# Kernel optimization log

Hardware: AMD Instinct MI355X
Metric: run time of the kernel (lower is better)

## Reference

```python
import jax, jax.numpy as jnp
import numpy as np

N_NODES = 50000
N_HEDGES = 10000
NNZ_INC = 400000
NNZ_E = 80000
NNZ_V = 400000
VDIM = 128
EDIM = 128
OUT_VDIM = 128
OUT_EDIM = 128


def _spmm(rows, cols, vals, X, n_rows):
    # sparse COO [n_rows, n_cols] @ X  -> [n_rows, d]
    return jax.ops.segment_sum(vals[:, None] * X[cols], rows, num_segments=n_rows)


def setup_inputs() -> dict:
    key = jax.random.key(0)
    ks = jax.random.split(key, 20)
    inp = {
        "vfeat": jax.random.normal(ks[0], (N_NODES, VDIM), jnp.float32),
        "efeat": jax.random.normal(ks[1], (N_HEDGES, EDIM), jnp.float32),
        "invDV": jax.random.uniform(ks[2], (N_NODES,), jnp.float32),
        "invDE": jax.random.uniform(ks[3], (N_HEDGES,), jnp.float32),
        "inc_src": jax.random.randint(ks[4], (NNZ_INC,), 0, N_NODES, jnp.int32),
        "inc_dst": jax.random.randint(ks[5], (NNZ_INC,), 0, N_HEDGES, jnp.int32),
        "emat_rows": jax.random.randint(ks[6], (NNZ_E,), 0, N_HEDGES, jnp.int32),
        "emat_cols": jax.random.randint(ks[7], (NNZ_E,), 0, N_HEDGES, jnp.int32),
        "emat_vals": jax.random.normal(ks[8], (NNZ_E,), jnp.float32),
        "vmat_rows": jax.random.randint(ks[9], (NNZ_V,), 0, N_NODES, jnp.int32),
        "vmat_cols": jax.random.randint(ks[10], (NNZ_V,), 0, N_NODES, jnp.int32),
        "vmat_vals": jax.random.normal(ks[11], (NNZ_V,), jnp.float32),
        # parameters (torch Linear: y = x @ W.T + b)
        "Wv": jax.random.normal(ks[12], (OUT_VDIM, VDIM), jnp.float32) * 0.05,
        "We": jax.random.normal(ks[13], (OUT_EDIM, EDIM), jnp.float32) * 0.05,
        "psi1_W": jax.random.normal(ks[14], (VDIM, VDIM + EDIM), jnp.float32) * 0.05,
        "psi1_b": jnp.zeros((VDIM,), jnp.float32),
        "psi2_W": jax.random.normal(ks[15], (EDIM, OUT_VDIM + EDIM), jnp.float32) * 0.05,
        "psi2_b": jnp.zeros((EDIM,), jnp.float32),
    }
    return inp


def reference(vfeat, efeat, invDV, invDE, inc_src, inc_dst,
              emat_rows, emat_cols, emat_vals,
              vmat_rows, vmat_cols, vmat_vals,
              Wv, We, psi1_W, psi1_b, psi2_W, psi2_b):
    N = vfeat.shape[0]
    E = efeat.shape[0]
    # --- 'in' update_all with psi1: per-incidence concat -> linear -> *invDV[src] -> sum into hyperedge
    x = jnp.concatenate([vfeat[inc_src], efeat[inc_dst]], axis=1)  # [nnz, VDIM+EDIM]
    x = x @ psi1_W.T + psi1_b                                       # [nnz, VDIM]
    x = x * invDV[inc_src][:, None]
    A = jax.ops.segment_sum(x, inc_dst, num_segments=E)             # [E, VDIM]
    A = _spmm(emat_rows, emat_cols, emat_vals, A, E)
    _efeat = A + efeat
    # --- 'con' update_all: node gathers sum of incident hyperedge feats
    _vfeat = jax.ops.segment_sum(_efeat[inc_dst], inc_src, num_segments=N)
    vfeat_out = jax.nn.relu(_vfeat @ Wv.T)                           # [N, OUT_VDIM]
    # --- 'in' update_all with psi2 (dv = ones)
    x2 = jnp.concatenate([vfeat_out[inc_src], efeat[inc_dst]], axis=1)
    x2 = x2 @ psi2_W.T + psi2_b                                      # [nnz, EDIM]
    B = jax.ops.segment_sum(x2, inc_dst, num_segments=E) * invDE[:, None]
    # --- 'con' pass with efeat, then vMat spmm, then 'in' sum back to hyperedges
    _vfeat2 = jax.ops.segment_sum(efeat[inc_dst], inc_src, num_segments=N)
    _vfeat2 = _spmm(vmat_rows, vmat_cols, vmat_vals, _vfeat2, N)
    _efeat2 = jax.ops.segment_sum(_vfeat2[inc_src], inc_dst, num_segments=E)
    _efeat2 = _efeat2 + B
    efeat_out = jax.nn.relu(_efeat2 @ We.T)                          # [E, OUT_EDIM]
    return vfeat_out, efeat_out
```

## Files before the change

### kernel.cpp

```cpp
#include <hip/hip_runtime.h>

#define NN 50000
#define NE 10000
#define NNZ_INC 400000
#define NNZ_E 80000
#define NNZ_V 400000
#define D 128
#define KC 32

#define CAP_D 112
#define CAP_S 40
#define CAP_E 40
#define CAP_V 40

#define NE_SH (NE / 8)
#define NN_SH (NN / 8)

#define GE_ 157
#define G_HINC ((NNZ_INC + 255) / 256)
#define G_HIST8 (8 * G_HINC)
#define G_EVB ((NNZ_E + NNZ_V + 255) / 256)
#define G_CVTN 6250
#define G_CVTE 1250
#define G_NR16 (NN / 16)
#define G_ER16 (NE / 16)

typedef unsigned short u16;
typedef unsigned int u32;

__device__ __forceinline__ u16 f2bf(float x) {
    unsigned u = __float_as_uint(x);
    unsigned r = u + 0x7fffu + ((u >> 16) & 1u);
    return (u16)(r >> 16);
}
__device__ __forceinline__ float bf2f(u16 h) {
    return __uint_as_float(((unsigned)h) << 16);
}

__device__ __forceinline__ void acc8(uint4 u, float acc[8]) {
    acc[0] += __uint_as_float(u.x << 16);
    acc[1] += __uint_as_float(u.x & 0xffff0000u);
    acc[2] += __uint_as_float(u.y << 16);
    acc[3] += __uint_as_float(u.y & 0xffff0000u);
    acc[4] += __uint_as_float(u.z << 16);
    acc[5] += __uint_as_float(u.z & 0xffff0000u);
    acc[6] += __uint_as_float(u.w << 16);
    acc[7] += __uint_as_float(u.w & 0xffff0000u);
}
__device__ __forceinline__ void fma8(uint4 u, float v, float acc[8]) {
    acc[0] = fmaf(v, __uint_as_float(u.x << 16), acc[0]);
    acc[1] = fmaf(v, __uint_as_float(u.x & 0xffff0000u), acc[1]);
    acc[2] = fmaf(v, __uint_as_float(u.y << 16), acc[2]);
    acc[3] = fmaf(v, __uint_as_float(u.y & 0xffff0000u), acc[3]);
    acc[4] = fmaf(v, __uint_as_float(u.z << 16), acc[4]);
    acc[5] = fmaf(v, __uint_as_float(u.z & 0xffff0000u), acc[5]);
    acc[6] = fmaf(v, __uint_as_float(u.w << 16), acc[6]);
    acc[7] = fmaf(v, __uint_as_float(u.w & 0xffff0000u), acc[7]);
}
__device__ __forceinline__ uint4 pack_bf8(const float acc[8]) {
    uint4 o;
    o.x = (u32)f2bf(acc[0]) | ((u32)f2bf(acc[1]) << 16);
    o.y = (u32)f2bf(acc[2]) | ((u32)f2bf(acc[3]) << 16);
    o.z = (u32)f2bf(acc[4]) | ((u32)f2bf(acc[5]) << 16);
    o.w = (u32)f2bf(acc[6]) | ((u32)f2bf(acc[7]) << 16);
    return o;
}

__device__ __forceinline__ void gemm_acc(
    int bx, const float* __restrict__ X, const float* __restrict__ W, int ldw,
    int M, float acc[8][4])
{
    __shared__ float XsT[KC][68];
    __shared__ float Ws[KC][132];
    const int tid = threadIdx.x;
    const int tx = tid & 31, ty = tid >> 5;
    const int row0 = bx * 64;
    const int c0 = tx * 4;
    const int r0 = ty * 8;

#pragma unroll
    for (int r = 0; r < 8; ++r)
#pragma unroll
        for (int c = 0; c < 4; ++c) acc[r][c] = 0.f;

    for (int kc = 0; kc < D; kc += KC) {
        __syncthreads();
#pragma unroll
        for (int it = 0; it < 2; ++it) {
            int l = tid + it * 256;
            int r = l >> 3, k4 = l & 7;
            float4 v = make_float4(0.f, 0.f, 0.f, 0.f);
            int row = row0 + r;
            if (row < M) v = ((const float4*)(X + (size_t)row * D + kc))[k4];
            int k = k4 * 4;
            XsT[k + 0][r] = v.x; XsT[k + 1][r] = v.y;
            XsT[k + 2][r] = v.z; XsT[k + 3][r] = v.w;
        }
#pragma unroll
        for (int it = 0; it < 4; ++it) {
            int l = tid + it * 256;
            int o = l >> 3, k4 = l & 7;
            float4 w = ((const float4*)(W + (size_t)o * ldw + kc))[k4];
            int k = k4 * 4;
            Ws[k + 0][o] = w.x; Ws[k + 1][o] = w.y;
            Ws[k + 2][o] = w.z; Ws[k + 3][o] = w.w;
        }
        __syncthreads();
#pragma unroll
        for (int k = 0; k < KC; ++k) {
            const float4 a0 = *(const float4*)&XsT[k][r0];
            const float4 a1 = *(const float4*)&XsT[k][r0 + 4];
            const float4 b  = *(const float4*)&Ws[k][c0];
            float av[8] = {a0.x, a0.y, a0.z, a0.w, a1.x, a1.y, a1.z, a1.w};
            float bv[4] = {b.x, b.y, b.z, b.w};
#pragma unroll
            for (int r = 0; r < 8; ++r)
#pragma unroll
                for (int c = 0; c < 4; ++c)
                    acc[r][c] = fmaf(av[r], bv[c], acc[r][c]);
        }
    }
}

__global__ __launch_bounds__(256) void mega0(
    const int* __restrict__ inc_src, const int* __restrict__ inc_dst,
    int* __restrict__ cnt_dst, int* __restrict__ cnt_src,
    u16* __restrict__ ell_d, u16* __restrict__ ell_s,
    const int* __restrict__ erows, const int* __restrict__ ecols,
    const float* __restrict__ evals, int* __restrict__ cnt_e, u32* __restrict__ ev_e,
    const int* __restrict__ vrows, const int* __restrict__ vcols,
    const float* __restrict__ vvals, int* __restrict__ cnt_v, u32* __restrict__ ev_v,
    const float* __restrict__ efeat, const float* __restrict__ vfeat,
    const float* __restrict__ invDV,
    u16* __restrict__ vfi_b, u16* __restrict__ efeat_b)
{
    int b = blockIdx.x;
    if (b < G_HIST8) {
        int shard = b & 7;
        int i = (b >> 3) * 256 + threadIdx.x;
        if (i < NNZ_INC) {
            int s = inc_src[i], d = inc_dst[i];
            if ((u32)(d - shard * NE_SH) < (u32)NE_SH) {
                int rd = atomicAdd(cnt_dst + d, 1);
                if (rd < CAP_D) ell_d[d * CAP_D + rd] = (u16)s;
            }
            if ((u32)(s - shard * NN_SH) < (u32)NN_SH) {
                int rs = atomicAdd(cnt_src + s, 1);
                if (rs < CAP_S) ell_s[s * CAP_S + rs] = (u16)d;
            }
        }
    } else if (b < G_HIST8 + G_EVB) {
        int i = (b - G_HIST8) * 256 + threadIdx.x;
        if (i < NNZ_E) {
            int r = erows[i];
            int re = atomicAdd(cnt_e + r, 1);
            if (re < CAP_E)
                ev_e[r * CAP_E + re] = ((u32)ecols[i] << 16) | (u32)f2bf(evals[i]);
        } else if (i < NNZ_E + NNZ_V) {
            int j = i - NNZ_E;
            int r = vrows[j];
            int rv = atomicAdd(cnt_v + r, 1);
            if (rv < CAP_V)
                ev_v[r * CAP_V + rv] = ((u32)vcols[j] << 16) | (u32)f2bf(vvals[j]);
        }
    } else if (b < G_HIST8 + G_EVB + G_CVTN) {
        int i = ((b - G_HIST8 - G_EVB) * 256 + threadIdx.x) * 4;
        int row = i >> 7;
        float s = invDV[row];
        float4 v = *(const float4*)(vfeat + i);
        ushort4 u;
        u.x = f2bf(v.x * s); u.y = f2bf(v.y * s);
        u.z = f2bf(v.z * s); u.w = f2bf(v.w * s);
        *(ushort4*)(vfi_b + i) = u;
    } else {
        int i = ((b - G_HIST8 - G_EVB - G_CVTN) * 256 + threadIdx.x) * 4;
        float4 v = *(const float4*)(efeat + i);
        ushort4 u;
        u.x = f2bf(v.x); u.y = f2bf(v.y); u.z = f2bf(v.z); u.w = f2bf(v.w);
        *(ushort4*)(efeat_b + i) = u;
    }
}

__device__ __forceinline__ void segsum_bf_ell16(int rb,
    const int* __restrict__ cnt, int cap, const u16* __restrict__ ell,
    const u16* __restrict__ Tb, u16* __restrict__ Yb, int R)
{
    int r = rb * 16 + (threadIdx.x >> 4);
    int q = threadIdx.x & 15;
    if (r >= R) return;
    int m = min(cnt[r], cap);
    const u16* lst = ell + (size_t)r * cap;
    float acc[8] = {0.f, 0.f, 0.f, 0.f, 0.f, 0.f, 0.f, 0.f};
    int j = 0;
    for (; j + 3 < m; j += 4) {
        ushort4 ix = *(const ushort4*)(lst + j);
        uint4 u0 = *(const uint4*)(Tb + (size_t)ix.x * D + q * 8);
        uint4 u1 = *(const uint4*)(Tb + (size_t)ix.y * D + q * 8);
        uint4 u2 = *(const uint4*)(Tb + (size_t)ix.z * D + q * 8);
        uint4 u3 = *(const uint4*)(Tb + (size_t)ix.w * D + q * 8);
        acc8(u0, acc); acc8(u1, acc); acc8(u2, acc); acc8(u3, acc);
    }
    for (; j < m; ++j) {
        uint4 u0 = *(const uint4*)(Tb + (size_t)lst[j] * D + q * 8);
        acc8(u0, acc);
    }
    ((uint4*)(Yb + (size_t)r * D))[q] = pack_bf8(acc);
}

__device__ __forceinline__ void segsum_f_ell16(int rb,
    const int* __restrict__ cnt, int cap, const u16* __restrict__ ell,
    const u16* __restrict__ Tb, float* __restrict__ Y, int R)
{
    int r = rb * 16 + (threadIdx.x >> 4);
    int q = threadIdx.x & 15;
    if (r >= R) return;
    int m = min(cnt[r], cap);
    const u16* lst = ell + (size_t)r * cap;
    float acc[8] = {0.f, 0.f, 0.f, 0.f, 0.f, 0.f, 0.f, 0.f};
    int j = 0;
    for (; j + 7 < m; j += 8) {
        ushort4 ixa = *(const ushort4*)(lst + j);
        ushort4 ixb = *(const ushort4*)(lst + j + 4);
        uint4 u0 = *(const uint4*)(Tb + (size_t)ixa.x * D + q * 8);
        uint4 u1 = *(const uint4*)(Tb + (size_t)ixa.y * D + q * 8);
        uint4 u2 = *(const uint4*)(Tb + (size_t)ixa.z * D + q * 8);
        uint4 u3 = *(const uint4*)(Tb + (size_t)ixa.w * D + q * 8);
        uint4 u4 = *(const uint4*)(Tb + (size_t)ixb.x * D + q * 8);
        uint4 u5 = *(const uint4*)(Tb + (size_t)ixb.y * D + q * 8);
        uint4 u6 = *(const uint4*)(Tb + (size_t)ixb.z * D + q * 8);
        uint4 u7 = *(const uint4*)(Tb + (size_t)ixb.w * D + q * 8);
        acc8(u0, acc); acc8(u1, acc); acc8(u2, acc); acc8(u3, acc);
        acc8(u4, acc); acc8(u5, acc); acc8(u6, acc); acc8(u7, acc);
    }
    for (; j + 3 < m; j += 4) {
        ushort4 ix = *(const ushort4*)(lst + j);
        uint4 u0 = *(const uint4*)(Tb + (size_t)ix.x * D + q * 8);
        uint4 u1 = *(const uint4*)(Tb + (size_t)ix.y * D + q * 8);
        uint4 u2 = *(const uint4*)(Tb + (size_t)ix.z * D + q * 8);
        uint4 u3 = *(const uint4*)(Tb + (size_t)ix.w * D + q * 8);
        acc8(u0, acc); acc8(u1, acc); acc8(u2, acc); acc8(u3, acc);
    }
    for (; j < m; ++j) {
        uint4 u0 = *(const uint4*)(Tb + (size_t)lst[j] * D + q * 8);
        acc8(u0, acc);
    }
    float* yr = Y + (size_t)r * D;
    ((float4*)yr)[2 * q + 0] = make_float4(acc[0], acc[1], acc[2], acc[3]);
    ((float4*)yr)[2 * q + 1] = make_float4(acc[4], acc[5], acc[6], acc[7]);
}

__device__ __forceinline__ void spmm_bf_ell16(int rb,
    const int* __restrict__ cnt, int cap, const u32* __restrict__ ell,
    const u16* __restrict__ Xb, const float* __restrict__ addend,
    u16* __restrict__ Yb, int R)
{
    int r = rb * 16 + (threadIdx.x >> 4);
    int q = threadIdx.x & 15;
    if (r >= R) return;
    int m = min(cnt[r], cap);
    const u32* lst = ell + (size_t)r * cap;
    float acc[8];
    if (addend) {
        const float* ar = addend + (size_t)r * D;
        float4 lo = ((const float4*)ar)[2 * q + 0];
        float4 hi = ((const float4*)ar)[2 * q + 1];
        acc[0] = lo.x; acc[1] = lo.y; acc[2] = lo.z; acc[3] = lo.w;
        acc[4] = hi.x; acc[5] = hi.y; acc[6] = hi.z; acc[7] = hi.w;
    } else {
#pragma unroll
        for (int i = 0; i < 8; ++i) acc[i] = 0.f;
    }
    int j = 0;
    for (; j + 3 < m; j += 4) {
        uint4 e = *(const uint4*)(lst + j);
        uint4 x0 = *(const uint4*)(Xb + (size_t)(e.x >> 16) * D + q * 8);
        uint4 x1 = *(const uint4*)(Xb + (size_t)(e.y >> 16) * D + q * 8);
        uint4 x2 = *(const uint4*)(Xb + (size_t)(e.z >> 16) * D + q * 8);
        uint4 x3 = *(const uint4*)(Xb + (size_t)(e.w >> 16) * D + q * 8);
        fma8(x0, __uint_as_float(e.x << 16), acc);
        fma8(x1, __uint_as_float(e.y << 16), acc);
        fma8(x2, __uint_as_float(e.z << 16), acc);
        fma8(x3, __uint_as_float(e.w << 16), acc);
    }
    for (; j < m; ++j) {
        u32 e = lst[j];
        uint4 x = *(const uint4*)(Xb + (size_t)(e >> 16) * D + q * 8);
        fma8(x, __uint_as_float(e << 16), acc);
    }
    ((uint4*)(Yb + (size_t)r * D))[q] = pack_bf8(acc);
}

__global__ __launch_bounds__(256) void fusedA(
    const float* __restrict__ efeat,
    const float* __restrict__ psi2_W, const float* __restrict__ psi2_b, float* __restrict__ QeP,
    const float* __restrict__ Wv, float* __restrict__ efP,
    const int* __restrict__ cnt_dst, const u16* __restrict__ ell_d,
    const float* __restrict__ invDV, const u16* __restrict__ vfi_b,
    float* __restrict__ sva, float* __restrict__ wsum,
    const int* __restrict__ cnt_src, const u16* __restrict__ ell_s,
    const u16* __restrict__ efeat_b, u16* __restrict__ vf2_b)
{
    int b = blockIdx.x;
    if (b < GE_) {
        float acc[8][4];
        gemm_acc(b, efeat, psi2_W + D, 2 * D, NE, acc);
        int tx = threadIdx.x & 31, ty = threadIdx.x >> 5;
        float4 b4 = ((const float4*)psi2_b)[tx];
#pragma unroll
        for (int r = 0; r < 8; ++r) {
            int row = b * 64 + ty * 8 + r;
            if (row < NE) {
                float4 v = make_float4(acc[r][0] + b4.x, acc[r][1] + b4.y,
                                       acc[r][2] + b4.z, acc[r][3] + b4.w);
                ((float4*)(QeP + (size_t)row * D))[tx] = v;
            }
        }
    } else if (b < 2 * GE_) {
        int bx = b - GE_;
        float acc[8][4];
        gemm_acc(bx, efeat, Wv, D, NE, acc);
        int tx = threadIdx.x & 31, ty = threadIdx.x >> 5;
#pragma unroll
        for (int r = 0; r < 8; ++r) {
            int row = bx * 64 + ty * 8 + r;
            if (row < NE) {
                float4 v = make_float4(acc[r][0], acc[r][1], acc[r][2], acc[r][3]);
                ((float4*)(efP + (size_t)row * D))[tx] = v;
            }
        }
    } else if (b < 2 * GE_ + G_ER16) {
        int e = (b - 2 * GE_) * 16 + (threadIdx.x >> 4);
        int q = threadIdx.x & 15;
        if (e >= NE) return;
        int m = min(cnt_dst[e], CAP_D);
        const u16* lst = ell_d + (size_t)e * CAP_D;
        float acc[8] = {0.f, 0.f, 0.f, 0.f, 0.f, 0.f, 0.f, 0.f};
        float ws = 0.f;
        int j = 0;
        for (; j + 3 < m; j += 4) {
            ushort4 ix = *(const ushort4*)(lst + j);
            uint4 u0 = *(const uint4*)(vfi_b + (size_t)ix.x * D + q * 8);
            uint4 u1 = *(const uint4*)(vfi_b + (size_t)ix.y * D + q * 8);
            uint4 u2 = *(const uint4*)(vfi_b + (size_t)ix.z * D + q * 8);
            uint4 u3 = *(const uint4*)(vfi_b + (size_t)ix.w * D + q * 8);
            ws += (invDV[ix.x] + invDV[ix.y]) + (invDV[ix.z] + invDV[ix.w]);
            acc8(u0, acc); acc8(u1, acc); acc8(u2, acc); acc8(u3, acc);
        }
        for (; j < m; ++j) {
            int s = lst[j];
            uint4 u0 = *(const uint4*)(vfi_b + (size_t)s * D + q * 8);
            ws += invDV[s];
            acc8(u0, acc);
        }
        float* yr = sva + (size_t)e * D;
        ((float4*)yr)[2 * q + 0] = make_float4(acc[0], acc[1], acc[2], acc[3]);
        ((float4*)yr)[2 * q + 1] = make_float4(acc[4], acc[5], acc[6], acc[7]);
        if (q == 0) wsum[e] = ws;
    } else {
        segsum_bf_ell16(b - 2 * GE_ - G_ER16, cnt_src, CAP_S, ell_s, efeat_b, vf2_b, NN);
    }
}

__global__ __launch_bounds__(256) void fusedB2(
    const float* __restrict__ sva, const float* __restrict__ efeat,
    const float* __restrict__ wsum,
    const float* __restrict__ psi1_W, const float* __restrict__ psi1_b,
    const float* __restrict__ Wv, u16* __restrict__ AP_b,
    const int* __restrict__ cnt_v, const u32* __restrict__ ev_v,
    const u16* __restrict__ vf2_b, u16* __restrict__ vf2b_b)
{
    int b = blockIdx.x;
    if (b >= GE_) {
        spmm_bf_ell16(b - GE_, cnt_v, CAP_V, ev_v, vf2_b, nullptr, vf2b_b, NN);
        return;
    }
    __shared__ float XsT[KC][68];
    __shared__ float Ws[KC][132];
    const int bx = b;
    const int tid = threadIdx.x;
    const int tx = tid & 31, ty = tid >> 5;
    const int row0 = bx * 64;
    const int c0 = tx * 4;
    const int r0 = ty * 8;
    float acc[8][4];
#pragma unroll
    for (int r = 0; r < 8; ++r)
#pragma unroll
        for (int c = 0; c < 4; ++c) acc[r][c] = 0.f;

    for (int kc = 0; kc < 2 * D; kc += KC) {
        __syncthreads();
        const bool second = (kc >= D);
        const float* Xp = second ? efeat : sva;
        const int kk = second ? kc - D : kc;
#pragma unroll
        for (int it = 0; it < 2; ++it) {
            int l = tid + it * 256;
            int r = l >> 3, k4 = l & 7;
            float4 v = make_float4(0.f, 0.f, 0.f, 0.f);
            int row = row0 + r;
            if (row < NE) {
                v = ((const float4*)(Xp + (size_t)row * D + kk))[k4];
                if (second) {
                    float sc = wsum[row];
                    v.x *= sc; v.y *= sc; v.z *= sc; v.w *= sc;
                }
            }
            int k = k4 * 4;
            XsT[k + 0][r] = v.x; XsT[k + 1][r] = v.y;
            XsT[k + 2][r] = v.z; XsT[k + 3][r] = v.w;
        }
#pragma unroll
        for (int it = 0; it < 4; ++it) {
            int l = tid + it * 256;
            int o = l >> 3, k4 = l & 7;
            float4 w = ((const float4*)(psi1_W + (size_t)o * (2 * D) + kc))[k4];
            int k = k4 * 4;
            Ws[k + 0][o] = w.x; Ws[k + 1][o] = w.y;
            Ws[k + 2][o] = w.z; Ws[k + 3][o] = w.w;
        }
        __syncthreads();
#pragma unroll
        for (int k = 0; k < KC; ++k) {
            const float4 a0 = *(const float4*)&XsT[k][r0];
            const float4 a1 = *(const float4*)&XsT[k][r0 + 4];
            const float4 bb = *(const float4*)&Ws[k][c0];
            float av[8] = {a0.x, a0.y, a0.z, a0.w, a1.x, a1.y, a1.z, a1.w};
            float bv[4] = {bb.x, bb.y, bb.z, bb.w};
#pragma unroll
            for (int r = 0; r < 8; ++r)
#pragma unroll
                for (int c = 0; c < 4; ++c)
                    acc[r][c] = fmaf(av[r], bv[c], acc[r][c]);
        }
    }
    float4 b4 = ((const float4*)psi1_b)[tx];
    float wsv[8];
#pragma unroll
    for (int r = 0; r < 8; ++r) {
        int row = row0 + r0 + r;
        wsv[r] = (row < NE) ? wsum[row] : 0.f;
    }
    float accP[8][4];
#pragma unroll
    for (int r = 0; r < 8; ++r)
#pragma unroll
        for (int c = 0; c < 4; ++c) accP[r][c] = 0.f;

    for (int kc = 0; kc < D; kc += KC) {
        __syncthreads();
        if ((u32)(tx - (kc >> 2)) < 8u) {
            int kk0 = tx * 4 - kc;
#pragma unroll
            for (int r = 0; r < 8; ++r) {
                XsT[kk0 + 0][r0 + r] = fmaf(wsv[r], b4.x, acc[r][0]);
                XsT[kk0 + 1][r0 + r] = fmaf(wsv[r], b4.y, acc[r][1]);
                XsT[kk0 + 2][r0 + r] = fmaf(wsv[r], b4.z, acc[r][2]);
                XsT[kk0 + 3][r0 + r] = fmaf(wsv[r], b4.w, acc[r][3]);
            }
        }
#pragma unroll
        for (int it = 0; it < 4; ++it) {
            int l = tid + it * 256;
            int o = l >> 3, k4 = l & 7;
            float4 w = ((const float4*)(Wv + (size_t)o * D + kc))[k4];
            int k = k4 * 4;
            Ws[k + 0][o] = w.x; Ws[k + 1][o] = w.y;
            Ws[k + 2][o] = w.z; Ws[k + 3][o] = w.w;
        }
        __syncthreads();
#pragma unroll
        for (int k = 0; k < KC; ++k) {
            const float4 a0 = *(const float4*)&XsT[k][r0];
            const float4 a1 = *(const float4*)&XsT[k][r0 + 4];
            const float4 bb = *(const float4*)&Ws[k][c0];
            float av[8] = {a0.x, a0.y, a0.z, a0.w, a1.x, a1.y, a1.z, a1.w};
            float bv[4] = {bb.x, bb.y, bb.z, bb.w};
#pragma unroll
            for (int r = 0; r < 8; ++r)
#pragma unroll
                for (int c = 0; c < 4; ++c)
                    accP[r][c] = fmaf(av[r], bv[c], accP[r][c]);
        }
    }
#pragma unroll
    for (int r = 0; r < 8; ++r) {
        int row = row0 + r0 + r;
        if (row < NE) {
            ushort4 u;
            u.x = f2bf(accP[r][0]); u.y = f2bf(accP[r][1]);
            u.z = f2bf(accP[r][2]); u.w = f2bf(accP[r][3]);
            ((ushort4*)(AP_b + (size_t)row * D))[tx] = u;
        }
    }
}

__global__ __launch_bounds__(256) void fusedC2(
    const int* __restrict__ cnt_dst, const u16* __restrict__ ell_d,
    const u16* __restrict__ vf2b_b, float* __restrict__ av,
    const int* __restrict__ cnt_e, const u32* __restrict__ ev_e,
    const u16* __restrict__ AP_b, const float* __restrict__ efP, u16* __restrict__ A2P_b)
{
    int b = blockIdx.x;
    if (b < G_ER16) segsum_f_ell16(b, cnt_dst, CAP_D, ell_d, vf2b_b, av, NE);
    else spmm_bf_ell16(b - G_ER16, cnt_e, CAP_E, ev_e, AP_b, efP, A2P_b, NE);
}

__global__ __launch_bounds__(256) void outv_k(
    const int* __restrict__ cnt_src, const u16* __restrict__ ell_s,
    const u16* __restrict__ A2P_b, float* __restrict__ out_v, u16* __restrict__ outv_b)
{
    int r = blockIdx.x * 16 + (threadIdx.x >> 4);
    int q = threadIdx.x & 15;
    if (r >= NN) return;
    int m = min(cnt_src[r], CAP_S);
    const u16* lst = ell_s + (size_t)r * CAP_S;
    float acc[8] = {0.f, 0.f, 0.f, 0.f, 0.f, 0.f, 0.f, 0.f};
    int j = 0;
    for (; j + 3 < m; j += 4) {
        ushort4 ix = *(const ushort4*)(lst + j);
        uint4 u0 = *(const uint4*)(A2P_b + (size_t)ix.x * D + q * 8);
        uint4 u1 = *(const uint4*)(A2P_b + (size_t)ix.y * D + q * 8);
        uint4 u2 = *(const uint4*)(A2P_b + (size_t)ix.z * D + q * 8);
        uint4 u3 = *(const uint4*)(A2P_b + (size_t)ix.w * D + q * 8);
        acc8(u0, acc); acc8(u1, acc); acc8(u2, acc); acc8(u3, acc);
    }
    for (; j < m; ++j) {
        uint4 u0 = *(const uint4*)(A2P_b + (size_t)lst[j] * D + q * 8);
        acc8(u0, acc);
    }
#pragma unroll
    for (int i = 0; i < 8; ++i) acc[i] = fmaxf(acc[i], 0.f);
    float* yr = out_v + (size_t)r * D;
    ((float4*)yr)[2 * q + 0] = make_float4(acc[0], acc[1], acc[2], acc[3]);
    ((float4*)yr)[2 * q + 1] = make_float4(acc[4], acc[5], acc[6], acc[7]);
    ((uint4*)(outv_b + (size_t)r * D))[q] = pack_bf8(acc);
}

__global__ __launch_bounds__(256) void gather_sv(
    const int* __restrict__ cnt_dst, const u16* __restrict__ ell_d,
    const u16* __restrict__ outv_b, float* __restrict__ sv)
{
    segsum_f_ell16(blockIdx.x, cnt_dst, CAP_D, ell_d, outv_b, sv, NE);
}

__global__ __launch_bounds__(256) void gemmBE_k(
    const float* __restrict__ sv, const float* __restrict__ psi2_W,
    const int* __restrict__ cnt_dst, const float* __restrict__ QeP,
    const float* __restrict__ invDE, const float* __restrict__ av,
    const float* __restrict__ We, float* __restrict__ out_e)
{
    __shared__ float T[D][68];
    float acc[8][4];
    gemm_acc(blockIdx.x, sv, psi2_W, 2 * D, NE, acc);
    const int tx = threadIdx.x & 31, ty = threadIdx.x >> 5;
    const int bx = blockIdx.x;
#pragma unroll
    for (int r = 0; r < 8; ++r) {
        int row = bx * 64 + ty * 8 + r;
        float deg = 0.f, ide = 0.f;
        float4 qe = make_float4(0.f, 0.f, 0.f, 0.f);
        float4 a  = make_float4(0.f, 0.f, 0.f, 0.f);
        if (row < NE) {
            deg = (float)cnt_dst[row];
            ide = invDE[row];
            qe = ((const float4*)(QeP + (size_t)row * D))[tx];
            a  = ((const float4*)(av  + (size_t)row * D))[tx];
        }
        int lr = ty * 8 + r;
        T[tx * 4 + 0][lr] = fmaf(deg, qe.x, acc[r][0]) * ide + a.x;
        T[tx * 4 + 1][lr] = fmaf(deg, qe.y, acc[r][1]) * ide + a.y;
        T[tx * 4 + 2][lr] = fmaf(deg, qe.z, acc[r][2]) * ide + a.z;
        T[tx * 4 + 3][lr] = fmaf(deg, qe.w, acc[r][3]) * ide + a.w;
    }
    __shared__ float Ws2[KC][132];
    float acc2[8][4];
#pragma unroll
    for (int r = 0; r < 8; ++r)
#pragma unroll
        for (int c = 0; c < 4; ++c) acc2[r][c] = 0.f;
    const int c0 = tx * 4, r0 = ty * 8;
    for (int kc = 0; kc < D; kc += KC) {
        __syncthreads();
#pragma unroll
        for (int it = 0; it < 4; ++it) {
            int l = threadIdx.x + it * 256;
            int o = l >> 3, k4 = l & 7;
            float4 w = ((const float4*)(We + (size_t)o * D + kc))[k4];
            int k = k4 * 4;
            Ws2[k + 0][o] = w.x; Ws2[k + 1][o] = w.y;
            Ws2[k + 2][o] = w.z; Ws2[k + 3][o] = w.w;
        }
        __syncthreads();
#pragma unroll
        for (int k = 0; k < KC; ++k) {
            const float4 a0 = *(const float4*)&T[kc + k][r0];
            const float4 a1 = *(const float4*)&T[kc + k][r0 + 4];
            const float4 bb = *(const float4*)&Ws2[k][c0];
            float avv[8] = {a0.x, a0.y, a0.z, a0.w, a1.x, a1.y, a1.z, a1.w};
            float bv[4] = {bb.x, bb.y, bb.z, bb.w};
#pragma unroll
            for (int r = 0; r < 8; ++r)
#pragma unroll
                for (int c = 0; c < 4; ++c)
                    acc2[r][c] = fmaf(avv[r], bv[c], acc2[r][c]);
        }
    }
#pragma unroll
    for (int r = 0; r < 8; ++r) {
        int row = bx * 64 + ty * 8 + r;
        if (row < NE) {
            float4 v = make_float4(fmaxf(acc2[r][0], 0.f), fmaxf(acc2[r][1], 0.f),
                                   fmaxf(acc2[r][2], 0.f), fmaxf(acc2[r][3], 0.f));
            ((float4*)(out_e + (size_t)row * D))[tx] = v;
        }
    }
}

extern "C" void kernel_launch(void* const* d_in, const int* in_sizes, int n_in,
                              void* d_out, int out_size, void* d_ws, size_t ws_size,
                              hipStream_t stream)
{
    (void)in_sizes; (void)n_in; (void)out_size; (void)ws_size;
    const float* vfeat     = (const float*)d_in[0];
    const float* efeat     = (const float*)d_in[1];
    const float* invDV     = (const float*)d_in[2];
    const float* invDE     = (const float*)d_in[3];
    const int*   inc_src   = (const int*)d_in[4];
    const int*   inc_dst   = (const int*)d_in[5];
    const int*   emat_rows = (const int*)d_in[6];
    const int*   emat_cols = (const int*)d_in[7];
    const float* emat_vals = (const float*)d_in[8];
    const int*   vmat_rows = (const int*)d_in[9];
    const int*   vmat_cols = (const int*)d_in[10];
    const float* vmat_vals = (const float*)d_in[11];
    const float* Wv        = (const float*)d_in[12];
    const float* We        = (const float*)d_in[13];
    const float* psi1_W    = (const float*)d_in[14];
    const float* psi1_b    = (const float*)d_in[15];
    const float* psi2_W    = (const float*)d_in[16];
    const float* psi2_b    = (const float*)d_in[17];

    const size_t ND = (size_t)NN * D;
    const size_t ED = (size_t)NE * D;

    char* p = (char*)d_ws;
    auto alloc = [&](size_t bytes) {
        size_t a = (size_t)p; a = (a + 255) & ~(size_t)255;
        p = (char*)a; void* r = (void*)p; p += bytes; return r;
    };
    float* QeP   = (float*)alloc(ED * 4);
    float* efP   = (float*)alloc(ED * 4);
    float* av    = (float*)alloc(ED * 4);
    float* svbuf = (float*)alloc(ED * 4);
    float* wsum  = (float*)alloc((size_t)NE * 4);
    u16* vfi_b   = (u16*)alloc(ND * 2);
    u16* outv_b  = (u16*)alloc(ND * 2);
    u16* vf2_b   = (u16*)alloc(ND * 2);
    u16* vf2b_b  = (u16*)alloc(ND * 2);
    u16* efeat_b = (u16*)alloc(ED * 2);
    u16* AP_b    = (u16*)alloc(ED * 2);
    u16* A2P_b   = (u16*)alloc(ED * 2);
    int* cnt_dst = (int*)alloc((size_t)(2 * NE + 2 * NN) * 4);
    int* cnt_src = cnt_dst + NE;
    int* cnt_e   = cnt_src + NN;
    int* cnt_v   = cnt_e + NE;
    u16* ell_d   = (u16*)alloc((size_t)NE * CAP_D * 2);
    u16* ell_s   = (u16*)alloc((size_t)NN * CAP_S * 2);
    u32* ev_e    = (u32*)alloc((size_t)NE * CAP_E * 4);
    u32* ev_v    = (u32*)alloc((size_t)NN * CAP_V * 4);

    float* out_v = (float*)d_out;
    float* out_e = out_v + ND;

    dim3 b256(256);

    hipMemsetAsync(cnt_dst, 0, (size_t)(2 * NE + 2 * NN) * sizeof(int), stream);
    mega0<<<G_HIST8 + G_EVB + G_CVTN + G_CVTE, b256, 0, stream>>>(
        inc_src, inc_dst, cnt_dst, cnt_src, ell_d, ell_s,
        emat_rows, emat_cols, emat_vals, cnt_e, ev_e,
        vmat_rows, vmat_cols, vmat_vals, cnt_v, ev_v,
        efeat, vfeat, invDV, vfi_b, efeat_b);
    fusedA<<<2 * GE_ + G_ER16 + G_NR16, b256, 0, stream>>>(
        efeat, psi2_W, psi2_b, QeP, Wv, efP,
        cnt_dst, ell_d, invDV, vfi_b, svbuf, wsum,
        cnt_src, ell_s, efeat_b, vf2_b);
    fusedB2<<<GE_ + G_NR16, b256, 0, stream>>>(
        svbuf, efeat, wsum, psi1_W, psi1_b, Wv, AP_b,
        cnt_v, ev_v, vf2_b, vf2b_b);
    fusedC2<<<G_ER16 + G_ER16, b256, 0, stream>>>(
        cnt_dst, ell_d, vf2b_b, av,
        cnt_e, ev_e, AP_b, efP, A2P_b);
    outv_k<<<G_NR16, b256, 0, stream>>>(cnt_src, ell_s, A2P_b, out_v, outv_b);
    gather_sv<<<G_ER16, b256, 0, stream>>>(cnt_dst, ell_d, outv_b, svbuf);
    gemmBE_k<<<GE_, b256, 0, stream>>>(svbuf, psi2_W, cnt_dst, QeP, invDE, av, We, out_e);
}
```

Measured before the change: 335.2 us.

## Rebalance work across fused kernels by moving COO bucketing and dense GEMMs

```diff
diff --git a/kernel.cpp b/kernel.cpp
--- a/kernel.cpp
+++ b/kernel.cpp
@@ -126,10 +126,6 @@
     const int* __restrict__ inc_src, const int* __restrict__ inc_dst,
     int* __restrict__ cnt_dst, int* __restrict__ cnt_src,
     u16* __restrict__ ell_d, u16* __restrict__ ell_s,
-    const int* __restrict__ erows, const int* __restrict__ ecols,
-    const float* __restrict__ evals, int* __restrict__ cnt_e, u32* __restrict__ ev_e,
-    const int* __restrict__ vrows, const int* __restrict__ vcols,
-    const float* __restrict__ vvals, int* __restrict__ cnt_v, u32* __restrict__ ev_v,
     const float* __restrict__ efeat, const float* __restrict__ vfeat,
     const float* __restrict__ invDV,
     u16* __restrict__ vfi_b, u16* __restrict__ efeat_b)
@@ -149,22 +145,8 @@
                 if (rs < CAP_S) ell_s[s * CAP_S + rs] = (u16)d;
             }
         }
-    } else if (b < G_HIST8 + G_EVB) {
-        int i = (b - G_HIST8) * 256 + threadIdx.x;
-        if (i < NNZ_E) {
-            int r = erows[i];
-            int re = atomicAdd(cnt_e + r, 1);
-            if (re < CAP_E)
-                ev_e[r * CAP_E + re] = ((u32)ecols[i] << 16) | (u32)f2bf(evals[i]);
-        } else if (i < NNZ_E + NNZ_V) {
-            int j = i - NNZ_E;
-            int r = vrows[j];
-            int rv = atomicAdd(cnt_v + r, 1);
-            if (rv < CAP_V)
-                ev_v[r * CAP_V + rv] = ((u32)vcols[j] << 16) | (u32)f2bf(vvals[j]);
-        }
-    } else if (b < G_HIST8 + G_EVB + G_CVTN) {
-        int i = ((b - G_HIST8 - G_EVB) * 256 + threadIdx.x) * 4;
+    } else if (b < G_HIST8 + G_CVTN) {
+        int i = ((b - G_HIST8) * 256 + threadIdx.x) * 4;
         int row = i >> 7;
         float s = invDV[row];
         float4 v = *(const float4*)(vfeat + i);
@@ -173,7 +155,7 @@
         u.z = f2bf(v.z * s); u.w = f2bf(v.w * s);
         *(ushort4*)(vfi_b + i) = u;
     } else {
-        int i = ((b - G_HIST8 - G_EVB - G_CVTN) * 256 + threadIdx.x) * 4;
+        int i = ((b - G_HIST8 - G_CVTN) * 256 + threadIdx.x) * 4;
         float4 v = *(const float4*)(efeat + i);
         ushort4 u;
         u.x = f2bf(v.x); u.y = f2bf(v.y); u.z = f2bf(v.z); u.w = f2bf(v.w);
@@ -291,9 +273,10 @@
 }
 
 __global__ __launch_bounds__(256) void fusedA(
-    const float* __restrict__ efeat,
-    const float* __restrict__ psi2_W, const float* __restrict__ psi2_b, float* __restrict__ QeP,
-    const float* __restrict__ Wv, float* __restrict__ efP,
+    const int* __restrict__ erows, const int* __restrict__ ecols,
+    const float* __restrict__ evals, int* __restrict__ cnt_e, u32* __restrict__ ev_e,
+    const int* __restrict__ vrows, const int* __restrict__ vcols,
+    const float* __restrict__ vvals, int* __restrict__ cnt_v, u32* __restrict__ ev_v,
     const int* __restrict__ cnt_dst, const u16* __restrict__ ell_d,
     const float* __restrict__ invDV, const u16* __restrict__ vfi_b,
     float* __restrict__ sva, float* __restrict__ wsum,
@@ -301,35 +284,22 @@
     const u16* __restrict__ efeat_b, u16* __restrict__ vf2_b)
 {
     int b = blockIdx.x;
-    if (b < GE_) {
-        float acc[8][4];
-        gemm_acc(b, efeat, psi2_W + D, 2 * D, NE, acc);
-        int tx = threadIdx.x & 31, ty = threadIdx.x >> 5;
-        float4 b4 = ((const float4*)psi2_b)[tx];
-#pragma unroll
-        for (int r = 0; r < 8; ++r) {
-            int row = b * 64 + ty * 8 + r;
-            if (row < NE) {
-                float4 v = make_float4(acc[r][0] + b4.x, acc[r][1] + b4.y,
-                                       acc[r][2] + b4.z, acc[r][3] + b4.w);
-                ((float4*)(QeP + (size_t)row * D))[tx] = v;
-            }
-        }
-    } else if (b < 2 * GE_) {
-        int bx = b - GE_;
-        float acc[8][4];
-        gemm_acc(bx, efeat, Wv, D, NE, acc);
-        int tx = threadIdx.x & 31, ty = threadIdx.x >> 5;
-#pragma unroll
-        for (int r = 0; r < 8; ++r) {
-            int row = bx * 64 + ty * 8 + r;
-            if (row < NE) {
-                float4 v = make_float4(acc[r][0], acc[r][1], acc[r][2], acc[r][3]);
-                ((float4*)(efP + (size_t)row * D))[tx] = v;
-            }
-        }
-    } else if (b < 2 * GE_ + G_ER16) {
-        int e = (b - 2 * GE_) * 16 + (threadIdx.x >> 4);
+    if (b < G_EVB) {
+        int i = b * 256 + threadIdx.x;
+        if (i < NNZ_E) {
+            int r = erows[i];
+            int re = atomicAdd(cnt_e + r, 1);
+            if (re < CAP_E)
+                ev_e[r * CAP_E + re] = ((u32)ecols[i] << 16) | (u32)f2bf(evals[i]);
+        } else if (i < NNZ_E + NNZ_V) {
+            int j = i - NNZ_E;
+            int r = vrows[j];
+            int rv = atomicAdd(cnt_v + r, 1);
+            if (rv < CAP_V)
+                ev_v[r * CAP_V + rv] = ((u32)vcols[j] << 16) | (u32)f2bf(vvals[j]);
+        }
+    } else if (b < G_EVB + G_ER16) {
+        int e = (b - G_EVB) * 16 + (threadIdx.x >> 4);
         int q = threadIdx.x & 15;
         if (e >= NE) return;
         int m = min(cnt_dst[e], CAP_D);
@@ -357,7 +327,7 @@
         ((float4*)yr)[2 * q + 1] = make_float4(acc[4], acc[5], acc[6], acc[7]);
         if (q == 0) wsum[e] = ws;
     } else {
-        segsum_bf_ell16(b - 2 * GE_ - G_ER16, cnt_src, CAP_S, ell_s, efeat_b, vf2_b, NN);
+        segsum_bf_ell16(b - G_EVB - G_ER16, cnt_src, CAP_S, ell_s, efeat_b, vf2_b, NN);
     }
 }
 
@@ -366,12 +336,46 @@
     const float* __restrict__ wsum,
     const float* __restrict__ psi1_W, const float* __restrict__ psi1_b,
     const float* __restrict__ Wv, u16* __restrict__ AP_b,
+    const float* __restrict__ psi2_W, const float* __restrict__ psi2_b,
+    float* __restrict__ QeP, float* __restrict__ efP,
     const int* __restrict__ cnt_v, const u32* __restrict__ ev_v,
     const u16* __restrict__ vf2_b, u16* __restrict__ vf2b_b)
 {
     int b = blockIdx.x;
+    if (b >= 3 * GE_) {
+        spmm_bf_ell16(b - 3 * GE_, cnt_v, CAP_V, ev_v, vf2_b, nullptr, vf2b_b, NN);
+        return;
+    }
     if (b >= GE_) {
-        spmm_bf_ell16(b - GE_, cnt_v, CAP_V, ev_v, vf2_b, nullptr, vf2b_b, NN);
+        if (b < 2 * GE_) {
+            int bx = b - GE_;
+            float acc[8][4];
+            gemm_acc(bx, efeat, psi2_W + D, 2 * D, NE, acc);
+            int tx = threadIdx.x & 31, ty = threadIdx.x >> 5;
+            float4 b4 = ((const float4*)psi2_b)[tx];
+#pragma unroll
+            for (int r = 0; r < 8; ++r) {
+                int row = bx * 64 + ty * 8 + r;
+                if (row < NE) {
+                    float4 v = make_float4(acc[r][0] + b4.x, acc[r][1] + b4.y,
+                                           acc[r][2] + b4.z, acc[r][3] + b4.w);
+                    ((float4*)(QeP + (size_t)row * D))[tx] = v;
+                }
+            }
+        } else {
+            int bx = b - 2 * GE_;
+            float acc[8][4];
+            gemm_acc(bx, efeat, Wv, D, NE, acc);
+            int tx = threadIdx.x & 31, ty = threadIdx.x >> 5;
+#pragma unroll
+            for (int r = 0; r < 8; ++r) {
+                int row = bx * 64 + ty * 8 + r;
+                if (row < NE) {
+                    float4 v = make_float4(acc[r][0], acc[r][1], acc[r][2], acc[r][3]);
+                    ((float4*)(efP + (size_t)row * D))[tx] = v;
+                }
+            }
+        }
         return;
     }
     __shared__ float XsT[KC][68];
@@ -676,17 +680,17 @@
     dim3 b256(256);
 
     hipMemsetAsync(cnt_dst, 0, (size_t)(2 * NE + 2 * NN) * sizeof(int), stream);
-    mega0<<<G_HIST8 + G_EVB + G_CVTN + G_CVTE, b256, 0, stream>>>(
+    mega0<<<G_HIST8 + G_CVTN + G_CVTE, b256, 0, stream>>>(
         inc_src, inc_dst, cnt_dst, cnt_src, ell_d, ell_s,
+        efeat, vfeat, invDV, vfi_b, efeat_b);
+    fusedA<<<G_EVB + G_ER16 + G_NR16, b256, 0, stream>>>(
         emat_rows, emat_cols, emat_vals, cnt_e, ev_e,
         vmat_rows, vmat_cols, vmat_vals, cnt_v, ev_v,
-        efeat, vfeat, invDV, vfi_b, efeat_b);
-    fusedA<<<2 * GE_ + G_ER16 + G_NR16, b256, 0, stream>>>(
-        efeat, psi2_W, psi2_b, QeP, Wv, efP,
         cnt_dst, ell_d, invDV, vfi_b, svbuf, wsum,
         cnt_src, ell_s, efeat_b, vf2_b);
-    fusedB2<<<GE_ + G_NR16, b256, 0, stream>>>(
+    fusedB2<<<3 * GE_ + G_NR16, b256, 0, stream>>>(
         svbuf, efeat, wsum, psi1_W, psi1_b, Wv, AP_b,
+        psi2_W, psi2_b, QeP, efP,
         cnt_v, ev_v, vf2_b, vf2b_b);
     fusedC2<<<G_ER16 + G_ER16, b256, 0, stream>>>(
         cnt_dst, ell_d, vf2b_b, av,
```

Measured after the change: 384.7 us. +14.8%, slower.
